# Optimization experiments

Measured on AMD Instinct MI355X. Metric: run time of the kernel, lower is better.

## Reference

```python
import jax, jax.numpy as jnp
import numpy as np

B, S, H, A = 16, 2048, 1024, 8


def setup_inputs() -> dict:
    key = jax.random.key(0)
    k1, k2, k3, k4 = jax.random.split(key, 4)
    token_embeddings = jax.random.normal(k1, (B, S, H), dtype=jnp.float32)
    aspect_embedding = jax.random.normal(k2, (B, A, H), dtype=jnp.float32)
    # Linear(2H -> H): stored as [2H, H] so we can use x @ W (same math as torch W^T)
    W = jax.random.normal(k3, (2 * H, H), dtype=jnp.float32) * (1.0 / np.sqrt(2 * H))
    b = jnp.zeros((H,), dtype=jnp.float32)
    v = jax.random.uniform(k4, (H,), dtype=jnp.float32)  # torch.rand init
    return {"token_embeddings": token_embeddings, "aspect_embedding": aspect_embedding,
            "W": W, "b": b, "v": v}


def reference(token_embeddings, aspect_embedding, W, b, v):
    # mean-pool aspect tokens -> [B, 1, H], broadcast over seq
    asp = jnp.mean(aspect_embedding, axis=1, keepdims=True)
    asp = jnp.broadcast_to(asp, token_embeddings.shape)          # [B, S, H]
    combined = jnp.concatenate([token_embeddings, asp], axis=2)   # [B, S, 2H]
    energy = jnp.tanh(combined @ W + b)                           # [B, S, H]
    scores = jnp.einsum('bsh,h->bs', energy, v)                   # [B, S]
    weights = jax.nn.softmax(scores, axis=1)                      # [B, S]
    # token * weights + token  ==  token * (1 + weights)
    return token_embeddings * (1.0 + weights[:, :, None])
```

## Files before the change

kernel.cpp:

```cpp
#include <hip/hip_runtime.h>
#include <hip/hip_bf16.h>
#include <stdint.h>


#define SEQ 2048
#define H 1024
#define MTOT 32768
#define BK 32

typedef __bf16 bf16x8 __attribute__((ext_vector_type(8)));
typedef float  f32x4  __attribute__((ext_vector_type(4)));

__device__ __forceinline__ void async16(const void* g, void* l) {
  __builtin_amdgcn_global_load_lds(
      (const __attribute__((address_space(1))) unsigned*)g,
      (__attribute__((address_space(3))) unsigned*)l, 16, 0, 0);
}

__device__ __forceinline__ unsigned f2bfraw(float f) {
  unsigned x = __float_as_uint(f);
  return (x + 0x7fffu + ((x >> 16) & 1u)) >> 16;
}
__device__ __forceinline__ unsigned pk2(float x, float y) {
  return f2bfraw(x) | (f2bfraw(y) << 16);
}
__device__ __forceinline__ float fast_tanh(float x) {
  x = fminf(fmaxf(x, -40.0f), 40.0f);
  float e = __expf(2.0f * x);
  return 1.0f - 2.0f / (e + 1.0f);
}

__global__ __launch_bounds__(256) void prep_k(
    const float* __restrict__ W,
    const float* __restrict__ asp,
    const float* __restrict__ bias,
    unsigned short* __restrict__ WT,
    float* __restrict__ cpart) {
  __shared__ __align__(16) float shbuf[1312];
  const int t = threadIdx.x;
  if (blockIdx.x < 1024) {
    float (*tile)[33] = reinterpret_cast<float(*)[33]>(shbuf);
    const int x = t & 31, y = t >> 5;
    const int n0 = (blockIdx.x & 31) * 32, k0 = (blockIdx.x >> 5) * 32;
#pragma unroll
    for (int i = 0; i < 4; ++i)
      tile[y + 8 * i][x] = W[(size_t)(k0 + y + 8 * i) * H + n0 + x];
    __syncthreads();
#pragma unroll
    for (int i = 0; i < 4; ++i)
      WT[(size_t)(n0 + y + 8 * i) * H + k0 + x] =
          (unsigned short)f2bfraw(tile[x][y + 8 * i]);
  } else {
    const int idx = blockIdx.x - 1024;
    const int b = idx & 15, nc = (idx >> 4) & 3, kc = idx >> 6;
    const int lane = t & 63, w = t >> 6;
    float* am = shbuf;
    f32x4* red = reinterpret_cast<f32x4*>(shbuf + 256);
    {
      const int k = kc * 256 + t;
      float s = 0.f;
#pragma unroll
      for (int a = 0; a < 8; ++a) s += asp[(size_t)(b * 8 + a) * H + k];
      am[t] = s * 0.125f;
    }
    __syncthreads();
    const int n = nc * 256 + lane * 4;
    const float* wp = W + (size_t)(H + kc * 256 + w * 64) * H + n;
    f32x4 acc = {};
#pragma unroll 8
    for (int k = 0; k < 64; ++k) {
      const f32x4 wv = *reinterpret_cast<const f32x4*>(wp + (size_t)k * H);
      const float a = am[w * 64 + k];
      acc[0] += a * wv[0]; acc[1] += a * wv[1];
      acc[2] += a * wv[2]; acc[3] += a * wv[3];
    }
    red[w * 64 + lane] = acc;
    __syncthreads();
    if (w == 0) {
      f32x4 r = red[lane];
#pragma unroll
      for (int i = 1; i < 4; ++i) {
        const f32x4 x = red[i * 64 + lane];
        r[0] += x[0]; r[1] += x[1]; r[2] += x[2]; r[3] += x[3];
      }
      if (kc == 0) {
        r[0] += bias[n];     r[1] += bias[n + 1];
        r[2] += bias[n + 2]; r[3] += bias[n + 3];
      }
      *reinterpret_cast<f32x4*>(cpart + (size_t)kc * 16 * H + b * H + n) = r;
    }
  }
}

__global__ __launch_bounds__(256) void gemm_score(
    const float* __restrict__ tokf,
    const __hip_bfloat16* __restrict__ wt,
    const float* __restrict__ cpart,
    const float* __restrict__ v,
    float* __restrict__ part) {
  __shared__ __hip_bfloat16 As[128 * BK];
  __shared__ __hip_bfloat16 Bs[128 * BK];
  const int t = threadIdx.x;
  const int lane = t & 63;
  const int w = t >> 6;
  const int wm = w >> 1, wn = w & 1;
  const unsigned bidl = blockIdx.x + (blockIdx.y << 3);
  const unsigned nb = ((bidl & 7u) << 8) | (bidl >> 3);
  const int bx = nb & 7;
  const int by = nb >> 3;
  const int m0 = by * 128;
  const int n0 = bx * 128;
  const int bb = by >> 4;

  f32x4 acc[4][4] = {};

  const int srow = t >> 2, scol = (t & 3) * 8;
  const float* ga = tokf + (size_t)(m0 + srow) * H + scol;
  const __hip_bfloat16* gb = wt + (size_t)(n0 + srow) * H + scol;
  __hip_bfloat16* la0 = As + t * 8;
  __hip_bfloat16* la1 = As + t * 8 + 64 * BK;
  __hip_bfloat16* lb0 = Bs + t * 8;
  __hip_bfloat16* lb1 = Bs + t * 8 + 64 * BK;

  const int quad = lane >> 4, l16 = lane & 15;

  f32x4 a0l = *reinterpret_cast<const f32x4*>(ga);
  f32x4 a0h = *reinterpret_cast<const f32x4*>(ga + 4);
  f32x4 a1l = *reinterpret_cast<const f32x4*>(ga + (size_t)64 * H);
  f32x4 a1h = *reinterpret_cast<const f32x4*>(ga + (size_t)64 * H + 4);

  for (int k0 = 0; k0 < H; k0 += BK) {
    __syncthreads();
    async16(gb + k0, lb0);
    async16(gb + k0 + (size_t)64 * H, lb1);
    uint4 r0, r1;
    r0.x = pk2(a0l[0], a0l[1]); r0.y = pk2(a0l[2], a0l[3]);
    r0.z = pk2(a0h[0], a0h[1]); r0.w = pk2(a0h[2], a0h[3]);
    r1.x = pk2(a1l[0], a1l[1]); r1.y = pk2(a1l[2], a1l[3]);
    r1.z = pk2(a1h[0], a1h[1]); r1.w = pk2(a1h[2], a1h[3]);
    *reinterpret_cast<uint4*>(la0) = r0;
    *reinterpret_cast<uint4*>(la1) = r1;
    __syncthreads();

    if (k0 + BK < H) {
      a0l = *reinterpret_cast<const f32x4*>(ga + k0 + BK);
      a0h = *reinterpret_cast<const f32x4*>(ga + k0 + BK + 4);
      a1l = *reinterpret_cast<const f32x4*>(ga + k0 + BK + (size_t)64 * H);
      a1h = *reinterpret_cast<const f32x4*>(ga + k0 + BK + (size_t)64 * H + 4);
    }

    bf16x8 af[4], bf[4];
#pragma unroll
    for (int mi = 0; mi < 4; ++mi)
      af[mi] = *reinterpret_cast<const bf16x8*>(
          As + (wm * 64 + mi * 16 + l16) * BK + quad * 8);
#pragma unroll
    for (int ni = 0; ni < 4; ++ni)
      bf[ni] = *reinterpret_cast<const bf16x8*>(
          Bs + (wn * 64 + ni * 16 + l16) * BK + quad * 8);
#pragma unroll
    for (int mi = 0; mi < 4; ++mi)
#pragma unroll
      for (int ni = 0; ni < 4; ++ni)
        acc[mi][ni] = __builtin_amdgcn_mfma_f32_16x16x32_bf16(
            af[mi], bf[ni], acc[mi][ni], 0, 0, 0);
  }

  float vv[4], cc[4];
#pragma unroll
  for (int ni = 0; ni < 4; ++ni) {
    const int gn = n0 + wn * 64 + ni * 16 + l16;
    vv[ni] = v[gn];
    float s = cpart[(size_t)bb * H + gn];
    s += cpart[(size_t)1 * 16 * H + bb * H + gn];
    s += cpart[(size_t)2 * 16 * H + bb * H + gn];
    s += cpart[(size_t)3 * 16 * H + bb * H + gn];
    cc[ni] = s;
  }
  const size_t pbase = ((size_t)bx * 2 + wn) * MTOT + m0;
#pragma unroll
  for (int mi = 0; mi < 4; ++mi) {
#pragma unroll
    for (int r = 0; r < 4; ++r) {
      float s = 0.f;
#pragma unroll
      for (int ni = 0; ni < 4; ++ni)
        s += fast_tanh(acc[mi][ni][r] + cc[ni]) * vv[ni];
#pragma unroll
      for (int msk = 1; msk < 16; msk <<= 1) s += __shfl_xor(s, msk, 64);
      if (l16 == 0)
        part[pbase + wm * 64 + mi * 16 + quad * 4 + r] = s;
    }
  }
}

__global__ __launch_bounds__(1024) void softmax_k(
    const float* __restrict__ part, float* __restrict__ wts) {
  const int b = blockIdx.x, t = threadIdx.x;
  const int lane = t & 63, w = t >> 6;
  __shared__ float red[16];
  const int s0 = t * 2;
  float sx = 0.f, sy = 0.f;
#pragma unroll
  for (int p = 0; p < 16; ++p) {
    const float2 x = *reinterpret_cast<const float2*>(
        part + (size_t)p * MTOT + b * SEQ + s0);
    sx += x.x; sy += x.y;
  }
  float m = fmaxf(sx, sy);
#pragma unroll
  for (int o = 1; o < 64; o <<= 1) m = fmaxf(m, __shfl_xor(m, o, 64));
  if (lane == 0) red[w] = m;
  __syncthreads();
  m = red[0];
#pragma unroll
  for (int i = 1; i < 16; ++i) m = fmaxf(m, red[i]);
  __syncthreads();
  const float e0 = __expf(sx - m), e1 = __expf(sy - m);
  float sum = e0 + e1;
#pragma unroll
  for (int o = 1; o < 64; o <<= 1) sum += __shfl_xor(sum, o, 64);
  if (lane == 0) red[w] = sum;
  __syncthreads();
  sum = 0.f;
#pragma unroll
  for (int i = 0; i < 16; ++i) sum += red[i];
  const float inv = 1.0f / sum;
  float2 o2; o2.x = e0 * inv; o2.y = e1 * inv;
  *reinterpret_cast<float2*>(wts + (size_t)b * SEQ + s0) = o2;
}

__global__ __launch_bounds__(256) void scale_k(
    const float* __restrict__ tok, const float* __restrict__ wts,
    float* __restrict__ out) {
  const size_t i = ((size_t)blockIdx.x * 256 + threadIdx.x) * 4;
  const float wm = 1.0f + wts[i >> 10];
  const f32x4 a = *reinterpret_cast<const f32x4*>(tok + i);
  f32x4 o;
  o[0] = a[0] * wm; o[1] = a[1] * wm; o[2] = a[2] * wm; o[3] = a[3] * wm;
  *reinterpret_cast<f32x4*>(out + i) = o;
}

extern "C" void kernel_launch(void* const* d_in, const int* in_sizes, int n_in,
                              void* d_out, int out_size, void* d_ws, size_t ws_size,
                              hipStream_t stream) {
  const float* tok  = (const float*)d_in[0];
  const float* asp  = (const float*)d_in[1];
  const float* W    = (const float*)d_in[2];
  const float* bias = (const float*)d_in[3];
  const float* v    = (const float*)d_in[4];
  float* out = (float*)d_out;

  float*          cpart  = out + 16777216;
  float*          part   = out + 32505856;
  unsigned short* WT_u   = (unsigned short*)(out + 33030144);
  float* wts = (ws_size >= (size_t)(SEQ * 16 * 4)) ? (float*)d_ws
                                                   : (float*)d_in[1];

  prep_k<<<1280, 256, 0, stream>>>(W, asp, bias, WT_u, cpart);
  gemm_score<<<dim3(8, 256), 256, 0, stream>>>(tok, (const __hip_bfloat16*)WT_u,
                                               cpart, v, part);
  softmax_k<<<16, 1024, 0, stream>>>(part, wts);
  scale_k<<<32768, 256, 0, stream>>>(tok, wts, out);
}
```

Measured before the change: 380.5 us.

## Pre-convert tokens to bf16 and double-buffer GEMM tiles with async LDS loads

Adds a prep pass that converts the fp32 token matrix to bf16 into scratch space (the first half of the output buffer). The GEMM then loads both A and B tiles with global-to-LDS async copies into a double-buffered shared array, so the next tile's load overlaps the current tile's MFMA work and each iteration needs one barrier instead of two. This removes the in-loop register conversion and the fp32 A loads eight times over, since eight N-blocks re-read each A tile. The cost is an extra 64MB read and 32MB write in the prep kernel, plus twice the LDS per block.

```diff
diff --git a/kernel.cpp b/kernel.cpp
--- a/kernel.cpp
+++ b/kernel.cpp
@@ -21,24 +21,33 @@
   unsigned x = __float_as_uint(f);
   return (x + 0x7fffu + ((x >> 16) & 1u)) >> 16;
 }
-__device__ __forceinline__ unsigned pk2(float x, float y) {
-  return f2bfraw(x) | (f2bfraw(y) << 16);
-}
 __device__ __forceinline__ float fast_tanh(float x) {
   x = fminf(fmaxf(x, -40.0f), 40.0f);
   float e = __expf(2.0f * x);
   return 1.0f - 2.0f / (e + 1.0f);
 }
 
-__global__ __launch_bounds__(256) void prep_k(
+__global__ __launch_bounds__(256) void prep_all(
     const float* __restrict__ W,
     const float* __restrict__ asp,
     const float* __restrict__ bias,
+    const float* __restrict__ tok,
     unsigned short* __restrict__ WT,
-    float* __restrict__ cpart) {
+    float* __restrict__ cpart,
+    unsigned short* __restrict__ tokb) {
   __shared__ __align__(16) float shbuf[1312];
   const int t = threadIdx.x;
-  if (blockIdx.x < 1024) {
+  if (blockIdx.x >= 1280) {
+    const size_t i = ((size_t)(blockIdx.x - 1280) * 256 + t) * 8;
+    const f32x4 a = *reinterpret_cast<const f32x4*>(tok + i);
+    const f32x4 b = *reinterpret_cast<const f32x4*>(tok + i + 4);
+    uint4 r;
+    r.x = f2bfraw(a[0]) | (f2bfraw(a[1]) << 16);
+    r.y = f2bfraw(a[2]) | (f2bfraw(a[3]) << 16);
+    r.z = f2bfraw(b[0]) | (f2bfraw(b[1]) << 16);
+    r.w = f2bfraw(b[2]) | (f2bfraw(b[3]) << 16);
+    *reinterpret_cast<uint4*>(tokb + i) = r;
+  } else if (blockIdx.x < 1024) {
     float (*tile)[33] = reinterpret_cast<float(*)[33]>(shbuf);
     const int x = t & 31, y = t >> 5;
     const int n0 = (blockIdx.x & 31) * 32, k0 = (blockIdx.x >> 5) * 32;
@@ -93,13 +102,12 @@
 }
 
 __global__ __launch_bounds__(256) void gemm_score(
-    const float* __restrict__ tokf,
+    const __hip_bfloat16* __restrict__ tokb,
     const __hip_bfloat16* __restrict__ wt,
     const float* __restrict__ cpart,
     const float* __restrict__ v,
     float* __restrict__ part) {
-  __shared__ __hip_bfloat16 As[128 * BK];
-  __shared__ __hip_bfloat16 Bs[128 * BK];
+  __shared__ __hip_bfloat16 lds[2 * 8192];
   const int t = threadIdx.x;
   const int lane = t & 63;
   const int w = t >> 6;
@@ -115,40 +123,21 @@
   f32x4 acc[4][4] = {};
 
   const int srow = t >> 2, scol = (t & 3) * 8;
-  const float* ga = tokf + (size_t)(m0 + srow) * H + scol;
+  const __hip_bfloat16* ga = tokb + (size_t)(m0 + srow) * H + scol;
   const __hip_bfloat16* gb = wt + (size_t)(n0 + srow) * H + scol;
-  __hip_bfloat16* la0 = As + t * 8;
-  __hip_bfloat16* la1 = As + t * 8 + 64 * BK;
-  __hip_bfloat16* lb0 = Bs + t * 8;
-  __hip_bfloat16* lb1 = Bs + t * 8 + 64 * BK;
-
   const int quad = lane >> 4, l16 = lane & 15;
 
-  f32x4 a0l = *reinterpret_cast<const f32x4*>(ga);
-  f32x4 a0h = *reinterpret_cast<const f32x4*>(ga + 4);
-  f32x4 a1l = *reinterpret_cast<const f32x4*>(ga + (size_t)64 * H);
-  f32x4 a1h = *reinterpret_cast<const f32x4*>(ga + (size_t)64 * H + 4);
-
-  for (int k0 = 0; k0 < H; k0 += BK) {
-    __syncthreads();
-    async16(gb + k0, lb0);
-    async16(gb + k0 + (size_t)64 * H, lb1);
-    uint4 r0, r1;
-    r0.x = pk2(a0l[0], a0l[1]); r0.y = pk2(a0l[2], a0l[3]);
-    r0.z = pk2(a0h[0], a0h[1]); r0.w = pk2(a0h[2], a0h[3]);
-    r1.x = pk2(a1l[0], a1l[1]); r1.y = pk2(a1l[2], a1l[3]);
-    r1.z = pk2(a1h[0], a1h[1]); r1.w = pk2(a1h[2], a1h[3]);
-    *reinterpret_cast<uint4*>(la0) = r0;
-    *reinterpret_cast<uint4*>(la1) = r1;
-    __syncthreads();
-
-    if (k0 + BK < H) {
-      a0l = *reinterpret_cast<const f32x4*>(ga + k0 + BK);
-      a0h = *reinterpret_cast<const f32x4*>(ga + k0 + BK + 4);
-      a1l = *reinterpret_cast<const f32x4*>(ga + k0 + BK + (size_t)64 * H);
-      a1h = *reinterpret_cast<const f32x4*>(ga + k0 + BK + (size_t)64 * H + 4);
-    }
-
+  auto stage = [&](int kt, int buf) {
+    __hip_bfloat16* p = lds + buf * 8192 + t * 8;
+    const int off = kt * BK;
+    async16(ga + off, p);
+    async16(ga + off + (size_t)64 * H, p + 2048);
+    async16(gb + off, p + 4096);
+    async16(gb + off + (size_t)64 * H, p + 4096 + 2048);
+  };
+  auto compute = [&](int buf) {
+    const __hip_bfloat16* As = lds + buf * 8192;
+    const __hip_bfloat16* Bs = As + 4096;
     bf16x8 af[4], bf[4];
 #pragma unroll
     for (int mi = 0; mi < 4; ++mi)
@@ -164,6 +153,15 @@
       for (int ni = 0; ni < 4; ++ni)
         acc[mi][ni] = __builtin_amdgcn_mfma_f32_16x16x32_bf16(
             af[mi], bf[ni], acc[mi][ni], 0, 0, 0);
+  };
+
+  stage(0, 0);
+  int cur = 0;
+  for (int kt = 0; kt < 32; ++kt) {
+    __syncthreads();
+    if (kt + 1 < 32) stage(kt + 1, cur ^ 1);
+    compute(cur);
+    cur ^= 1;
   }
 
   float vv[4], cc[4];
@@ -251,15 +249,17 @@
   const float* v    = (const float*)d_in[4];
   float* out = (float*)d_out;
 
+  unsigned short* tokb_u = (unsigned short*)out;
   float*          cpart  = out + 16777216;
   float*          part   = out + 32505856;
   unsigned short* WT_u   = (unsigned short*)(out + 33030144);
   float* wts = (ws_size >= (size_t)(SEQ * 16 * 4)) ? (float*)d_ws
                                                    : (float*)d_in[1];
 
-  prep_k<<<1280, 256, 0, stream>>>(W, asp, bias, WT_u, cpart);
-  gemm_score<<<dim3(8, 256), 256, 0, stream>>>(tok, (const __hip_bfloat16*)WT_u,
-                                               cpart, v, part);
+  prep_all<<<17664, 256, 0, stream>>>(W, asp, bias, tok, WT_u, cpart, tokb_u);
+  gemm_score<<<dim3(8, 256), 256, 0, stream>>>(
+      (const __hip_bfloat16*)tokb_u, (const __hip_bfloat16*)WT_u,
+      cpart, v, part);
   softmax_k<<<16, 1024, 0, stream>>>(part, wts);
   scale_k<<<32768, 256, 0, stream>>>(tok, wts, out);
 }
```

After: 363.1 us. 4.6% less time.
